# Optimization experiments

Measured on AMD Instinct MI355X. Metric: run time of the kernel, lower is better.

The kernel has to match this reference:

```python
import jax, jax.numpy as jnp
import numpy as np

DIM = 128
NUM_HEADS = 8
HEAD_DIM = DIM // NUM_HEADS
N_NODES = 50000
N_EDGES = 800000


def setup_inputs() -> dict:
    key = jax.random.key(0)
    ks = jax.random.split(key, 10)
    scale = 1.0 / np.sqrt(DIM)
    x = jax.random.normal(ks[0], (N_NODES, DIM), dtype=jnp.float32)
    edge_index = jax.random.randint(ks[1], (2, N_EDGES), 0, N_NODES, dtype=jnp.int64)
    Wq = jax.random.normal(ks[2], (DIM, DIM), dtype=jnp.float32) * scale
    bq = jnp.zeros((DIM,), dtype=jnp.float32)
    Wk = jax.random.normal(ks[3], (DIM, DIM), dtype=jnp.float32) * scale
    bk = jnp.zeros((DIM,), dtype=jnp.float32)
    Wv = jax.random.normal(ks[4], (DIM, DIM), dtype=jnp.float32) * scale
    bv = jnp.zeros((DIM,), dtype=jnp.float32)
    Wo = jax.random.normal(ks[5], (DIM, DIM), dtype=jnp.float32) * scale
    bo = jnp.zeros((DIM,), dtype=jnp.float32)
    return {"x": x, "edge_index": edge_index, "Wq": Wq, "bq": bq,
            "Wk": Wk, "bk": bk, "Wv": Wv, "bv": bv, "Wo": Wo, "bo": bo}


def reference(x, edge_index, Wq, bq, Wk, bk, Wv, bv, Wo, bo):
    n = x.shape[0]
    tgt = edge_index[0]  # softmax group / scatter destination
    src = edge_index[1]  # gather source
    # projections: torch nn.Linear -> x @ W.T + b
    q = (x @ Wq.T + bq).reshape(n, NUM_HEADS, HEAD_DIM)
    k = (x @ Wk.T + bk).reshape(n, NUM_HEADS, HEAD_DIM)
    v = (x @ Wv.T + bv).reshape(n, NUM_HEADS, HEAD_DIM)
    # edge-wise attention scores: [E, H]
    scores = jnp.einsum('ehd,ehd->eh', q[src], k[tgt]) / np.sqrt(HEAD_DIM).astype(np.float32)
    # segment softmax over edges grouped by target node
    m = jax.ops.segment_max(scores, tgt, num_segments=n)          # [N, H]
    m = jax.lax.stop_gradient(m)
    p = jnp.exp(scores - m[tgt])                                   # [E, H]
    s = jax.ops.segment_sum(p, tgt, num_segments=n)               # [N, H]
    probs = p / s[tgt]
    # weighted scatter-add of source values
    weighted = v[src] * probs[..., None]                           # [E, H, D]
    agg = jax.ops.segment_sum(weighted, tgt, num_segments=n)      # [N, H, D]
    out = agg.reshape(n, DIM) @ Wo.T + bo
    # dropout is identity in eval mode
    return out
```

## Files before the change

### kernel.cpp

```cpp
#include <hip/hip_runtime.h>
#include <hip/hip_bf16.h>
#include <math.h>

#define NN 50000
#define NE 800000
#define DIM 128
#define NH 8
#define HD 16
#define NTILE 3125
#define TPB 782
#define LROW 136
#define QVROW 256
#define SCAN_B 196

typedef short v8s __attribute__((ext_vector_type(8)));
typedef float v4f __attribute__((ext_vector_type(4)));

__device__ __forceinline__ unsigned pack2(float a, float b) {
    __hip_bfloat162 h = __float22bfloat162_rn(make_float2(a, b));
    return *reinterpret_cast<unsigned*>(&h);
}
__device__ __forceinline__ float blo(unsigned w) { return __uint_as_float(w << 16); }
__device__ __forceinline__ float bhi(unsigned w) { return __uint_as_float(w & 0xffff0000u); }

__device__ __forceinline__ void stage_w_lds(
    const float* __restrict__ Wg, unsigned short* __restrict__ Wl, int tid)
{
#pragma unroll
    for (int it = 0; it < 8; ++it) {
        int chunk = it * 256 + tid;
        int row = chunk >> 4, c8 = chunk & 15;
        float4 f0 = ((const float4*)Wg)[2 * chunk];
        float4 f1 = ((const float4*)Wg)[2 * chunk + 1];
        uint4 o = { pack2(f0.x, f0.y), pack2(f0.z, f0.w),
                    pack2(f1.x, f1.y), pack2(f1.z, f1.w) };
        *(uint4*)(Wl + row * LROW + c8 * 8) = o;
    }
}

__global__ __launch_bounds__(256) void qkv_mfma_kernel(
    const float* __restrict__ x,
    const float* __restrict__ Wq, const float* __restrict__ Wk, const float* __restrict__ Wv,
    const float* __restrict__ bq, const float* __restrict__ bk, const float* __restrict__ bv,
    unsigned short* __restrict__ qvb, unsigned short* __restrict__ kb,
    const int* __restrict__ tgt, int* __restrict__ cnt)
{
    __shared__ unsigned short Wl[DIM * LROW];
    const int tid = threadIdx.x;
    const int lane = tid & 63;
    const int warp = tid >> 6;
    const int m = lane & 15;
    const int quad = lane >> 4;

    const int gsize = TPB * 256;
    for (int e = blockIdx.x * 256 + tid; e < NE; e += gsize)
        atomicAdd(cnt + tgt[e], 1);

    const int rt = blockIdx.x * 4 + warp;
    const bool active = (rt < NTILE);
    const int node = (active ? rt : 0) * 16 + m;

    v8s a[4];
    if (active) {
#pragma unroll
        for (int kt = 0; kt < 4; ++kt) {
            const float4* xr = (const float4*)(x + (size_t)node * DIM + kt * 32 + quad * 8);
            float4 f0 = xr[0], f1 = xr[1];
            uint4 u = { pack2(f0.x, f0.y), pack2(f0.z, f0.w),
                        pack2(f1.x, f1.y), pack2(f1.z, f1.w) };
            a[kt] = *(v8s*)&u;
        }
    }

    stage_w_lds(Wq, Wl, tid);
    __syncthreads();
    uint2 uq[8];
    if (active) {
#pragma unroll
        for (int nt = 0; nt < 8; ++nt) {
            v4f c = {0.f, 0.f, 0.f, 0.f};
#pragma unroll
            for (int kt = 0; kt < 4; ++kt) {
                v8s wf = *(const v8s*)(Wl + (nt * 16 + m) * LROW + kt * 32 + quad * 8);
                c = __builtin_amdgcn_mfma_f32_16x16x32_bf16(wf, a[kt], c, 0, 0, 0);
            }
            int cbase = nt * 16 + quad * 4;
            float4 b4 = *(const float4*)(bq + cbase);
            uq[nt].x = pack2(c[0] + b4.x, c[1] + b4.y);
            uq[nt].y = pack2(c[2] + b4.z, c[3] + b4.w);
        }
    }
    __syncthreads();

    stage_w_lds(Wv, Wl, tid);
    __syncthreads();
    if (active) {
#pragma unroll
        for (int nt = 0; nt < 8; ++nt) {
            v4f c = {0.f, 0.f, 0.f, 0.f};
#pragma unroll
            for (int kt = 0; kt < 4; ++kt) {
                v8s wf = *(const v8s*)(Wl + (nt * 16 + m) * LROW + kt * 32 + quad * 8);
                c = __builtin_amdgcn_mfma_f32_16x16x32_bf16(wf, a[kt], c, 0, 0, 0);
            }
            int cbase = nt * 16 + quad * 4;
            float4 b4 = *(const float4*)(bv + cbase);
            unsigned v01 = pack2(c[0] + b4.x, c[1] + b4.y);
            unsigned v23 = pack2(c[2] + b4.z, c[3] + b4.w);
            uint4 st = { uq[nt].x, v01, uq[nt].y, v23 };
            *(uint4*)(qvb + (size_t)node * QVROW + 2 * cbase) = st;
        }
    }
    __syncthreads();

    stage_w_lds(Wk, Wl, tid);
    __syncthreads();
    if (active) {
#pragma unroll
        for (int nt = 0; nt < 8; ++nt) {
            v4f c = {0.f, 0.f, 0.f, 0.f};
#pragma unroll
            for (int kt = 0; kt < 4; ++kt) {
                v8s wf = *(const v8s*)(Wl + (nt * 16 + m) * LROW + kt * 32 + quad * 8);
                c = __builtin_amdgcn_mfma_f32_16x16x32_bf16(wf, a[kt], c, 0, 0, 0);
            }
            int cbase = nt * 16 + quad * 4;
            float4 b4 = *(const float4*)(bk + cbase);
            uint2 pk = { pack2(c[0] + b4.x, c[1] + b4.y),
                         pack2(c[2] + b4.z, c[3] + b4.w) };
            *(uint2*)(kb + (size_t)node * DIM + cbase) = pk;
        }
    }
}

__global__ __launch_bounds__(256) void scan1_kernel(
    const int* __restrict__ cnt, int* __restrict__ off, int* __restrict__ bsum)
{
    __shared__ int ws4[4];
    const int tid = threadIdx.x, lane = tid & 63, wid = tid >> 6;
    int i = blockIdx.x * 256 + tid;
    int v0 = (i < NN) ? cnt[i] : 0;
    int incl = v0;
#pragma unroll
    for (int d = 1; d < 64; d <<= 1) {
        int t = __shfl_up(incl, d);
        if (lane >= d) incl += t;
    }
    if (lane == 63) ws4[wid] = incl;
    __syncthreads();
    int wexcl = 0;
#pragma unroll
    for (int t = 0; t < 3; ++t) if (t < wid) wexcl += ws4[t];
    if (i < NN) off[i] = wexcl + incl - v0;
    if (tid == 255) bsum[blockIdx.x] = wexcl + incl;
}

__global__ __launch_bounds__(256) void scan23_kernel(
    const int* __restrict__ bsum, int* __restrict__ off, int* __restrict__ cursor)
{
    __shared__ int ws4[4];
    __shared__ int base_s, total_s;
    const int tid = threadIdx.x, lane = tid & 63, wid = tid >> 6;
    int v0 = (tid < SCAN_B) ? bsum[tid] : 0;
    int incl = v0;
#pragma unroll
    for (int d = 1; d < 64; d <<= 1) {
        int t = __shfl_up(incl, d);
        if (lane >= d) incl += t;
    }
    if (lane == 63) ws4[wid] = incl;
    __syncthreads();
    int wexcl = 0;
#pragma unroll
    for (int t = 0; t < 3; ++t) if (t < wid) wexcl += ws4[t];
    int excl = wexcl + incl - v0;
    if (tid == blockIdx.x) base_s = excl;
    if (tid == SCAN_B - 1) total_s = excl + v0;
    __syncthreads();
    int i = blockIdx.x * 256 + tid;
    if (i < NN) {
        int t = off[i] + base_s;
        off[i] = t;
        cursor[i] = t;
    }
    if (blockIdx.x == SCAN_B - 1 && tid == 0) off[NN] = total_s;
}

__global__ __launch_bounds__(256) void fill_kernel(
    const int* __restrict__ tgt, const int* __restrict__ src,
    int* __restrict__ cursor, int* __restrict__ edge_src)
{
    int e = blockIdx.x * 256 + threadIdx.x;
    if (e >= NE) return;
    int t = tgt[e];
    int pos = atomicAdd(cursor + t, 1);
    edge_src[pos] = src[e];
}

__global__ __launch_bounds__(256) void attn_kernel(
    const int* __restrict__ off, const int* __restrict__ edge_src,
    const unsigned short* __restrict__ qvb, const unsigned short* __restrict__ kb,
    unsigned short* __restrict__ aggb)
{
    __shared__ float red[2][64][3];
    const int tid = threadIdx.x;
    const int nib = tid >> 7;
    const int w   = (tid >> 6) & 1;
    const int lane = tid & 63;
    const int node = blockIdx.x * 2 + nib;

    const int base = off[node];
    const int deg  = off[node + 1] - base;

    unsigned kw = *(const unsigned*)(kb + (size_t)node * DIM + 2 * lane);
    const float klo = blo(kw), khi = bhi(kw);

    const int j = lane & 7;
    const int gb = lane & 56;

    float ax = 0.f, ay = 0.f, ss = 0.f;
    const int nw = (deg + 1 - w) >> 1;
    for (int c0 = 0; c0 < nw; c0 += 64) {
        int idx = c0 + lane;
        int srcv = edge_src[base + min(2 * idx + w, deg - 1)];
        int nchunk = min(nw - c0, 64);
        for (int b = 0; b < nchunk; b += 8) {
            int nb = min(nchunk - b, 8);
            uint2 qv[8];
#pragma unroll
            for (int i = 0; i < 8; ++i) {
                int si = __shfl(srcv, b + min(i, nb - 1));
                qv[i] = *(const uint2*)(qvb + (size_t)si * QVROW + 4 * lane);
            }
            float part[8];
#pragma unroll
            for (int i = 0; i < 8; ++i)
                part[i] = blo(qv[i].x) * klo + bhi(qv[i].x) * khi;
            float r1[4];
#pragma unroll
            for (int t = 0; t < 4; ++t) {
                float keep = (j & 1) ? part[2 * t + 1] : part[2 * t];
                float send = (j & 1) ? part[2 * t]     : part[2 * t + 1];
                r1[t] = keep + __shfl_xor(send, 1);
            }
            float r2[2];
#pragma unroll
            for (int u = 0; u < 2; ++u) {
                float keep = (j & 2) ? r1[2 * u + 1] : r1[2 * u];
                float send = (j & 2) ? r1[2 * u]     : r1[2 * u + 1];
                r2[u] = keep + __shfl_xor(send, 2);
            }
            float keep = (j & 4) ? r2[1] : r2[0];
            float send = (j & 4) ? r2[0] : r2[1];
            float tot = keep + __shfl_xor(send, 4);
            float p = __expf(tot * 0.25f);
#pragma unroll
            for (int i = 0; i < 8; ++i) {
                if (i < nb) {
                    float pi = __shfl(p, gb + i);
                    unsigned vv = qv[i].y;
                    ax += pi * blo(vv);
                    ay += pi * bhi(vv);
                    ss += pi;
                }
            }
        }
    }
    if (w == 1) {
        red[nib][lane][0] = ax; red[nib][lane][1] = ay; red[nib][lane][2] = ss;
    }
    __syncthreads();
    if (w == 0) {
        ax += red[nib][lane][0]; ay += red[nib][lane][1]; ss += red[nib][lane][2];
        unsigned* ap = (unsigned*)(aggb + (size_t)node * DIM + 2 * lane);
        if (deg == 0) {
            *ap = 0u;
        } else {
            float inv = 1.f / ss;
            *ap = pack2(ax * inv, ay * inv);
        }
    }
}

__global__ __launch_bounds__(256) void outproj_mfma_kernel(
    const unsigned short* __restrict__ aggb, const float* __restrict__ Wo,
    const float* __restrict__ bo, float* __restrict__ out)
{
    __shared__ unsigned short Wl[DIM * LROW];
    const int tid = threadIdx.x;
    const int lane = tid & 63;
    const int warp = tid >> 6;
    const int m = lane & 15;
    const int quad = lane >> 4;

    stage_w_lds(Wo, Wl, tid);

    const int rt = blockIdx.x * 4 + warp;
    const bool active = (rt < NTILE);
    const int node = (active ? rt : 0) * 16 + m;

    v8s a[4];
    if (active) {
#pragma unroll
        for (int kt = 0; kt < 4; ++kt)
            a[kt] = *(const v8s*)(aggb + (size_t)node * DIM + kt * 32 + quad * 8);
    }
    __syncthreads();
    if (!active) return;

#pragma unroll
    for (int nt = 0; nt < 8; ++nt) {
        v4f c = {0.f, 0.f, 0.f, 0.f};
#pragma unroll
        for (int kt = 0; kt < 4; ++kt) {
            v8s wf = *(const v8s*)(Wl + (nt * 16 + m) * LROW + kt * 32 + quad * 8);
            c = __builtin_amdgcn_mfma_f32_16x16x32_bf16(wf, a[kt], c, 0, 0, 0);
        }
        const int cbase = nt * 16 + quad * 4;
        float4 b4 = *(const float4*)(bo + cbase);
        float4 o = { c[0] + b4.x, c[1] + b4.y, c[2] + b4.z, c[3] + b4.w };
        *(float4*)(out + (size_t)node * DIM + cbase) = o;
    }
}

extern "C" void kernel_launch(void* const* d_in, const int* in_sizes, int n_in,
                              void* d_out, int out_size, void* d_ws, size_t ws_size,
                              hipStream_t stream) {
    const float* x  = (const float*)d_in[0];
    const int*   ei = (const int*)d_in[1];
    const float* Wq = (const float*)d_in[2];
    const float* bq = (const float*)d_in[3];
    const float* Wk = (const float*)d_in[4];
    const float* bk = (const float*)d_in[5];
    const float* Wv = (const float*)d_in[6];
    const float* bv = (const float*)d_in[7];
    const float* Wo = (const float*)d_in[8];
    const float* bo = (const float*)d_in[9];

    const int* tgt = ei;
    const int* src = ei + NE;

    char* ws = (char*)d_ws;
    const size_t SZ_QV = (size_t)NN * QVROW * 2;
    const size_t SZ_BF = (size_t)NN * DIM * 2;

    unsigned short* qvb  = (unsigned short*)(ws);
    unsigned short* kb   = (unsigned short*)(ws + SZ_QV);
    unsigned short* aggb = (unsigned short*)(ws + SZ_QV + SZ_BF);

    char* wi = ws + SZ_QV + 2 * SZ_BF;
    int* cnt      = (int*)(wi);
    int* off      = (int*)(wi + (size_t)NN * 4);
    int* cursor   = (int*)(wi + (size_t)(2 * NN + 1) * 4);
    int* edge_src = (int*)(wi + (size_t)(3 * NN + 1) * 4);
    int* bsum     = (int*)(wi + (size_t)(3 * NN + 1) * 4 + (size_t)NE * 4);

    const int edge_blocks = (NE + 255) / 256;

    hipMemsetAsync(cnt, 0, (size_t)NN * 4, stream);
    qkv_mfma_kernel<<<TPB, 256, 0, stream>>>(
        x, Wq, Wk, Wv, bq, bk, bv, qvb, kb, tgt, cnt);
    scan1_kernel<<<SCAN_B, 256, 0, stream>>>(cnt, off, bsum);
    scan23_kernel<<<SCAN_B, 256, 0, stream>>>(bsum, off, cursor);
    fill_kernel<<<edge_blocks, 256, 0, stream>>>(tgt, src, cursor, edge_src);
    attn_kernel<<<(NN + 1) / 2, 256, 0, stream>>>(off, edge_src, qvb, kb, aggb);
    outproj_mfma_kernel<<<TPB, 256, 0, stream>>>(aggb, Wo, bo, (float*)d_out);
}
```

Measured before the change: 258.8 us.

## Merge CSR build into cooperative kernel and drop LDS weight staging in QKV

Moves the memset, degree counting, two-level scan and CSR fill into one cooperative kernel with grid-wide syncs, replacing four launches and taking the tgt atomics out of the QKV kernel. The QKV kernel now reads weight fragments straight from global memory, no longer stages weights in LDS or uses block barriers, and assembles interleaved q/v rows in a swizzled LDS buffer so stores are coalesced. This cuts launch and barrier overhead but serialises the CSR build onto only 256 blocks and repeats bf16 conversion of the weights in every warp.

Measured after the change: 459.1 us. 1.77x slower.

```diff
diff --git a/kernel.cpp b/kernel.cpp
--- a/kernel.cpp
+++ b/kernel.cpp
@@ -1,6 +1,9 @@
 #include <hip/hip_runtime.h>
 #include <hip/hip_bf16.h>
+#include <hip/hip_cooperative_groups.h>
 #include <math.h>
+
+namespace cg = cooperative_groups;
 
 #define NN 50000
 #define NE 800000
@@ -12,6 +15,7 @@
 #define LROW 136
 #define QVROW 256
 #define SCAN_B 196
+#define CSRB 256
 
 typedef short v8s __attribute__((ext_vector_type(8)));
 typedef float v4f __attribute__((ext_vector_type(4)));
@@ -23,178 +27,164 @@
 __device__ __forceinline__ float blo(unsigned w) { return __uint_as_float(w << 16); }
 __device__ __forceinline__ float bhi(unsigned w) { return __uint_as_float(w & 0xffff0000u); }
 
-__device__ __forceinline__ void stage_w_lds(
-    const float* __restrict__ Wg, unsigned short* __restrict__ Wl, int tid)
-{
-#pragma unroll
-    for (int it = 0; it < 8; ++it) {
-        int chunk = it * 256 + tid;
-        int row = chunk >> 4, c8 = chunk & 15;
-        float4 f0 = ((const float4*)Wg)[2 * chunk];
-        float4 f1 = ((const float4*)Wg)[2 * chunk + 1];
-        uint4 o = { pack2(f0.x, f0.y), pack2(f0.z, f0.w),
-                    pack2(f1.x, f1.y), pack2(f1.z, f1.w) };
-        *(uint4*)(Wl + row * LROW + c8 * 8) = o;
-    }
-}
-
-__global__ __launch_bounds__(256) void qkv_mfma_kernel(
+__device__ __forceinline__ v8s wfrag(const float* __restrict__ W, int row, int koff) {
+    const float4* wr = (const float4*)(W + (size_t)row * DIM + koff);
+    float4 f0 = wr[0], f1 = wr[1];
+    uint4 u = { pack2(f0.x, f0.y), pack2(f0.z, f0.w),
+                pack2(f1.x, f1.y), pack2(f1.z, f1.w) };
+    return *(v8s*)&u;
+}
+
+__global__ __launch_bounds__(256) void qkv_kernel(
     const float* __restrict__ x,
     const float* __restrict__ Wq, const float* __restrict__ Wk, const float* __restrict__ Wv,
     const float* __restrict__ bq, const float* __restrict__ bk, const float* __restrict__ bv,
-    unsigned short* __restrict__ qvb, unsigned short* __restrict__ kb,
-    const int* __restrict__ tgt, int* __restrict__ cnt)
-{
-    __shared__ unsigned short Wl[DIM * LROW];
+    unsigned short* __restrict__ qvb, unsigned short* __restrict__ kb)
+{
+    __shared__ unsigned qvstage[4][16][128];
     const int tid = threadIdx.x;
     const int lane = tid & 63;
     const int warp = tid >> 6;
     const int m = lane & 15;
     const int quad = lane >> 4;
 
-    const int gsize = TPB * 256;
-    for (int e = blockIdx.x * 256 + tid; e < NE; e += gsize)
-        atomicAdd(cnt + tgt[e], 1);
-
     const int rt = blockIdx.x * 4 + warp;
-    const bool active = (rt < NTILE);
-    const int node = (active ? rt : 0) * 16 + m;
+    if (rt >= NTILE) return;
+    const int node = rt * 16 + m;
 
     v8s a[4];
-    if (active) {
-#pragma unroll
-        for (int kt = 0; kt < 4; ++kt) {
-            const float4* xr = (const float4*)(x + (size_t)node * DIM + kt * 32 + quad * 8);
-            float4 f0 = xr[0], f1 = xr[1];
-            uint4 u = { pack2(f0.x, f0.y), pack2(f0.z, f0.w),
-                        pack2(f1.x, f1.y), pack2(f1.z, f1.w) };
-            a[kt] = *(v8s*)&u;
-        }
-    }
-
-    stage_w_lds(Wq, Wl, tid);
-    __syncthreads();
-    uint2 uq[8];
-    if (active) {
-#pragma unroll
-        for (int nt = 0; nt < 8; ++nt) {
-            v4f c = {0.f, 0.f, 0.f, 0.f};
-#pragma unroll
-            for (int kt = 0; kt < 4; ++kt) {
-                v8s wf = *(const v8s*)(Wl + (nt * 16 + m) * LROW + kt * 32 + quad * 8);
-                c = __builtin_amdgcn_mfma_f32_16x16x32_bf16(wf, a[kt], c, 0, 0, 0);
-            }
-            int cbase = nt * 16 + quad * 4;
-            float4 b4 = *(const float4*)(bq + cbase);
-            uq[nt].x = pack2(c[0] + b4.x, c[1] + b4.y);
-            uq[nt].y = pack2(c[2] + b4.z, c[3] + b4.w);
-        }
-    }
-    __syncthreads();
-
-    stage_w_lds(Wv, Wl, tid);
-    __syncthreads();
-    if (active) {
-#pragma unroll
-        for (int nt = 0; nt < 8; ++nt) {
-            v4f c = {0.f, 0.f, 0.f, 0.f};
-#pragma unroll
-            for (int kt = 0; kt < 4; ++kt) {
-                v8s wf = *(const v8s*)(Wl + (nt * 16 + m) * LROW + kt * 32 + quad * 8);
-                c = __builtin_amdgcn_mfma_f32_16x16x32_bf16(wf, a[kt], c, 0, 0, 0);
-            }
-            int cbase = nt * 16 + quad * 4;
-            float4 b4 = *(const float4*)(bv + cbase);
-            unsigned v01 = pack2(c[0] + b4.x, c[1] + b4.y);
-            unsigned v23 = pack2(c[2] + b4.z, c[3] + b4.w);
-            uint4 st = { uq[nt].x, v01, uq[nt].y, v23 };
-            *(uint4*)(qvb + (size_t)node * QVROW + 2 * cbase) = st;
-        }
-    }
-    __syncthreads();
-
-    stage_w_lds(Wk, Wl, tid);
-    __syncthreads();
-    if (active) {
-#pragma unroll
-        for (int nt = 0; nt < 8; ++nt) {
-            v4f c = {0.f, 0.f, 0.f, 0.f};
-#pragma unroll
-            for (int kt = 0; kt < 4; ++kt) {
-                v8s wf = *(const v8s*)(Wl + (nt * 16 + m) * LROW + kt * 32 + quad * 8);
-                c = __builtin_amdgcn_mfma_f32_16x16x32_bf16(wf, a[kt], c, 0, 0, 0);
-            }
-            int cbase = nt * 16 + quad * 4;
-            float4 b4 = *(const float4*)(bk + cbase);
-            uint2 pk = { pack2(c[0] + b4.x, c[1] + b4.y),
-                         pack2(c[2] + b4.z, c[3] + b4.w) };
-            *(uint2*)(kb + (size_t)node * DIM + cbase) = pk;
-        }
-    }
-}
-
-__global__ __launch_bounds__(256) void scan1_kernel(
-    const int* __restrict__ cnt, int* __restrict__ off, int* __restrict__ bsum)
-{
-    __shared__ int ws4[4];
-    const int tid = threadIdx.x, lane = tid & 63, wid = tid >> 6;
-    int i = blockIdx.x * 256 + tid;
-    int v0 = (i < NN) ? cnt[i] : 0;
-    int incl = v0;
-#pragma unroll
-    for (int d = 1; d < 64; d <<= 1) {
-        int t = __shfl_up(incl, d);
-        if (lane >= d) incl += t;
-    }
-    if (lane == 63) ws4[wid] = incl;
-    __syncthreads();
-    int wexcl = 0;
-#pragma unroll
-    for (int t = 0; t < 3; ++t) if (t < wid) wexcl += ws4[t];
-    if (i < NN) off[i] = wexcl + incl - v0;
-    if (tid == 255) bsum[blockIdx.x] = wexcl + incl;
-}
-
-__global__ __launch_bounds__(256) void scan23_kernel(
-    const int* __restrict__ bsum, int* __restrict__ off, int* __restrict__ cursor)
-{
+#pragma unroll
+    for (int kt = 0; kt < 4; ++kt) {
+        const float4* xr = (const float4*)(x + (size_t)node * DIM + kt * 32 + quad * 8);
+        float4 f0 = xr[0], f1 = xr[1];
+        uint4 u = { pack2(f0.x, f0.y), pack2(f0.z, f0.w),
+                    pack2(f1.x, f1.y), pack2(f1.z, f1.w) };
+        a[kt] = *(v8s*)&u;
+    }
+
+#pragma unroll
+    for (int nt = 0; nt < 8; ++nt) {
+        v4f c = {0.f, 0.f, 0.f, 0.f};
+#pragma unroll
+        for (int kt = 0; kt < 4; ++kt)
+            c = __builtin_amdgcn_mfma_f32_16x16x32_bf16(
+                    wfrag(Wk, nt * 16 + m, kt * 32 + quad * 8), a[kt], c, 0, 0, 0);
+        int cbase = nt * 16 + quad * 4;
+        float4 b4 = *(const float4*)(bk + cbase);
+        uint2 pk = { pack2(c[0] + b4.x, c[1] + b4.y),
+                     pack2(c[2] + b4.z, c[3] + b4.w) };
+        *(uint2*)(kb + (size_t)node * DIM + cbase) = pk;
+    }
+
+#pragma unroll
+    for (int nt = 0; nt < 8; ++nt) {
+        v4f c = {0.f, 0.f, 0.f, 0.f};
+#pragma unroll
+        for (int kt = 0; kt < 4; ++kt)
+            c = __builtin_amdgcn_mfma_f32_16x16x32_bf16(
+                    wfrag(Wq, nt * 16 + m, kt * 32 + quad * 8), a[kt], c, 0, 0, 0);
+        int cbase = nt * 16 + quad * 4;
+        float4 b4 = *(const float4*)(bq + cbase);
+        unsigned* up = &qvstage[warp][m][(((nt * 4 + quad) ^ m) & 31) * 4];
+        up[0] = pack2(c[0] + b4.x, c[1] + b4.y);
+        up[2] = pack2(c[2] + b4.z, c[3] + b4.w);
+    }
+
+#pragma unroll
+    for (int nt = 0; nt < 8; ++nt) {
+        v4f c = {0.f, 0.f, 0.f, 0.f};
+#pragma unroll
+        for (int kt = 0; kt < 4; ++kt)
+            c = __builtin_amdgcn_mfma_f32_16x16x32_bf16(
+                    wfrag(Wv, nt * 16 + m, kt * 32 + quad * 8), a[kt], c, 0, 0, 0);
+        int cbase = nt * 16 + quad * 4;
+        float4 b4 = *(const float4*)(bv + cbase);
+        unsigned* up = &qvstage[warp][m][(((nt * 4 + quad) ^ m) & 31) * 4];
+        up[1] = pack2(c[0] + b4.x, c[1] + b4.y);
+        up[3] = pack2(c[2] + b4.z, c[3] + b4.w);
+    }
+
+    const int r0 = rt * 16;
+#pragma unroll
+    for (int i = 0; i < 8; ++i) {
+        int chunk = i * 64 + lane;
+        int row = chunk >> 5;
+        int c16 = chunk & 31;
+        uint4 val = *(uint4*)&qvstage[warp][row][((c16 ^ row) & 31) * 4];
+        *(uint4*)(qvb + (size_t)(r0 + row) * QVROW + c16 * 8) = val;
+    }
+}
+
+__global__ __launch_bounds__(256) void csr_kernel(
+    const int* __restrict__ tgt, const int* __restrict__ src,
+    int* __restrict__ cnt, int* __restrict__ off, int* __restrict__ cursor,
+    int* __restrict__ edge_src, int* __restrict__ bsum)
+{
+    cg::grid_group grid = cg::this_grid();
     __shared__ int ws4[4];
     __shared__ int base_s, total_s;
-    const int tid = threadIdx.x, lane = tid & 63, wid = tid >> 6;
-    int v0 = (tid < SCAN_B) ? bsum[tid] : 0;
-    int incl = v0;
-#pragma unroll
-    for (int d = 1; d < 64; d <<= 1) {
-        int t = __shfl_up(incl, d);
-        if (lane >= d) incl += t;
-    }
-    if (lane == 63) ws4[wid] = incl;
-    __syncthreads();
-    int wexcl = 0;
-#pragma unroll
-    for (int t = 0; t < 3; ++t) if (t < wid) wexcl += ws4[t];
-    int excl = wexcl + incl - v0;
-    if (tid == blockIdx.x) base_s = excl;
-    if (tid == SCAN_B - 1) total_s = excl + v0;
-    __syncthreads();
-    int i = blockIdx.x * 256 + tid;
-    if (i < NN) {
-        int t = off[i] + base_s;
-        off[i] = t;
-        cursor[i] = t;
-    }
-    if (blockIdx.x == SCAN_B - 1 && tid == 0) off[NN] = total_s;
-}
-
-__global__ __launch_bounds__(256) void fill_kernel(
-    const int* __restrict__ tgt, const int* __restrict__ src,
-    int* __restrict__ cursor, int* __restrict__ edge_src)
-{
-    int e = blockIdx.x * 256 + threadIdx.x;
-    if (e >= NE) return;
-    int t = tgt[e];
-    int pos = atomicAdd(cursor + t, 1);
-    edge_src[pos] = src[e];
+    const int tid = threadIdx.x, bid = blockIdx.x;
+    const int lane = tid & 63, wid = tid >> 6;
+    const int gtid = bid * 256 + tid, gsz = CSRB * 256;
+
+    for (int i = gtid; i < NN; i += gsz) cnt[i] = 0;
+    grid.sync();
+
+    for (int e = gtid; e < NE; e += gsz) atomicAdd(cnt + tgt[e], 1);
+    grid.sync();
+
+    {
+        int i = gtid;
+        int v0 = (i < NN) ? cnt[i] : 0;
+        int incl = v0;
+#pragma unroll
+        for (int d = 1; d < 64; d <<= 1) {
+            int t = __shfl_up(incl, d);
+            if (lane >= d) incl += t;
+        }
+        if (lane == 63) ws4[wid] = incl;
+        __syncthreads();
+        int wexcl = 0;
+#pragma unroll
+        for (int t = 0; t < 3; ++t) if (t < wid) wexcl += ws4[t];
+        if (i < NN) off[i] = wexcl + incl - v0;
+        if (tid == 255 && bid < SCAN_B) bsum[bid] = wexcl + incl;
+    }
+    grid.sync();
+
+    {
+        __syncthreads();
+        int v0 = (tid < SCAN_B) ? bsum[tid] : 0;
+        int incl = v0;
+#pragma unroll
+        for (int d = 1; d < 64; d <<= 1) {
+            int t = __shfl_up(incl, d);
+            if (lane >= d) incl += t;
+        }
+        if (lane == 63) ws4[wid] = incl;
+        __syncthreads();
+        int wexcl = 0;
+#pragma unroll
+        for (int t = 0; t < 3; ++t) if (t < wid) wexcl += ws4[t];
+        int excl = wexcl + incl - v0;
+        if (tid == bid) base_s = excl;
+        if (tid == SCAN_B - 1) total_s = excl + v0;
+        __syncthreads();
+        int i = gtid;
+        if (i < NN) {
+            int t = off[i] + base_s;
+            off[i] = t;
+            cursor[i] = t;
+        }
+        if (bid == SCAN_B - 1 && tid == 0) off[NN] = total_s;
+    }
+    grid.sync();
+
+    for (int e = gtid; e < NE; e += gsz) {
+        int t = tgt[e];
+        int pos = atomicAdd(cursor + t, 1);
+        edge_src[pos] = src[e];
+    }
 }
 
 __global__ __launch_bounds__(256) void attn_kernel(
@@ -279,6 +269,21 @@
             float inv = 1.f / ss;
             *ap = pack2(ax * inv, ay * inv);
         }
+    }
+}
+
+__device__ __forceinline__ void stage_w_lds(
+    const float* __restrict__ Wg, unsigned short* __restrict__ Wl, int tid)
+{
+#pragma unroll
+    for (int it = 0; it < 8; ++it) {
+        int chunk = it * 256 + tid;
+        int row = chunk >> 4, c8 = chunk & 15;
+        float4 f0 = ((const float4*)Wg)[2 * chunk];
+        float4 f1 = ((const float4*)Wg)[2 * chunk + 1];
+        uint4 o = { pack2(f0.x, f0.y), pack2(f0.z, f0.w),
+                    pack2(f1.x, f1.y), pack2(f1.z, f1.w) };
+        *(uint4*)(Wl + row * LROW + c8 * 8) = o;
     }
 }
 
@@ -355,14 +360,14 @@
     int* edge_src = (int*)(wi + (size_t)(3 * NN + 1) * 4);
     int* bsum     = (int*)(wi + (size_t)(3 * NN + 1) * 4 + (size_t)NE * 4);
 
-    const int edge_blocks = (NE + 255) / 256;
-
-    hipMemsetAsync(cnt, 0, (size_t)NN * 4, stream);
-    qkv_mfma_kernel<<<TPB, 256, 0, stream>>>(
-        x, Wq, Wk, Wv, bq, bk, bv, qvb, kb, tgt, cnt);
-    scan1_kernel<<<SCAN_B, 256, 0, stream>>>(cnt, off, bsum);
-    scan23_kernel<<<SCAN_B, 256, 0, stream>>>(bsum, off, cursor);
-    fill_kernel<<<edge_blocks, 256, 0, stream>>>(tgt, src, cursor, edge_src);
+    qkv_kernel<<<TPB, 256, 0, stream>>>(
+        x, Wq, Wk, Wv, bq, bk, bv, qvb, kb);
+
+    void* csr_args[] = { (void*)&tgt, (void*)&src, (void*)&cnt, (void*)&off,
+                         (void*)&cursor, (void*)&edge_src, (void*)&bsum };
+    hipLaunchCooperativeKernel((void*)csr_kernel, dim3(CSRB), dim3(256),
+                               csr_args, 0, stream);
+
     attn_kernel<<<(NN + 1) / 2, 256, 0, stream>>>(off, edge_src, qvb, kb, aggb);
     outproj_mfma_kernel<<<TPB, 256, 0, stream>>>(aggb, Wo, bo, (float*)d_out);
 }
```
